# Performance work log

Measured on AMD Instinct MI355X. Metric: run time of the kernel, lower is better.

## Reference

```python
import jax, jax.numpy as jnp
import numpy as np

NUM_HEADS = 16
SRC_FACTS = 4


def setup_inputs() -> dict:
    key = jax.random.key(0)
    k1, k2, k3, k4, k5 = jax.random.split(key, 5)
    B, S, H, Dh = 16, 512, NUM_HEADS, 64  # B = batch(4) * src_facts(4)
    D = H * Dh  # d_model = 1024
    pre_q = jax.random.normal(k1, (B, S, H, Dh), dtype=jnp.float32)
    pre_v = jax.random.normal(k2, (B, S, H, Dh), dtype=jnp.float32)
    pre_k = jax.random.normal(k3, (B, S, H, Dh), dtype=jnp.float32)
    attn_mask = jax.random.randint(k4, (B, S, S), 0, 2).astype(jnp.int32)
    output_weights = jax.random.normal(k5, (D, D), dtype=jnp.float32) / np.float32(np.sqrt(D))
    return {
        "pre_q": pre_q,
        "pre_v": pre_v,
        "pre_k": pre_k,
        "attn_mask": attn_mask,
        "output_weights": output_weights,
        "out_seq_len": 512,
        "d_model": 1024,
    }


def reference(pre_q, pre_v, pre_k, attn_mask, output_weights, out_seq_len, d_model):
    B, Sq, H, Dh = pre_q.shape
    # Original: K.sqrt(cast(d_model) // num_heads) -> sqrt(head_dim)
    scale = jnp.sqrt(jnp.float32(float(d_model) // H))
    mask = attn_mask.astype(jnp.float32)[:, None]  # (B, 1, q, k) broadcast over heads
    # scores: (B, H, q, k)
    scores = jnp.einsum("bqhd,bkhd->bhqk", pre_q, pre_k) / scale
    # multiplicative pre-mask + additive -1e9 on masked slots
    scores = scores * mask + (1.0 - mask) * jnp.float32(-1e9)
    # softmax then multiplicative post-mask
    attn = jax.nn.softmax(scores, axis=-1) * mask
    heads = jnp.einsum("bhqk,bkhd->bqhd", attn, pre_v)  # (B, q, H, Dh)
    out = heads.reshape(B, Sq, H * Dh) @ output_weights  # (B, q, d_model)
    return out.reshape(-1, SRC_FACTS, out_seq_len, d_model)
```

## Files before the change

### kernel.cpp

```cpp
#include <hip/hip_runtime.h>
#include <hip/hip_bf16.h>


typedef __bf16 bf16;
typedef bf16 bf16x8 __attribute__((ext_vector_type(8)));
typedef bf16 bf16x4 __attribute__((ext_vector_type(4)));
typedef float floatx4 __attribute__((ext_vector_type(4)));
typedef float floatx16 __attribute__((ext_vector_type(16)));
typedef unsigned short ushort8 __attribute__((ext_vector_type(8)));
typedef unsigned long long u64;

#define MFMA32(A, B, C)    __builtin_amdgcn_mfma_f32_16x16x32_bf16((A), (B), (C), 0, 0, 0)
#define MFMA32x32(A, B, C) __builtin_amdgcn_mfma_f32_32x32x16_bf16((A), (B), (C), 0, 0, 0)

namespace {
constexpr int S    = 512;
constexpr int H    = 16;
constexpr int Dh   = 64;
constexpr int D    = 1024;
constexpr int LDT  = 72;
constexpr int LDTV = 136;
constexpr size_t QN = (size_t)16 * S * H * Dh;
constexpr size_t WN = (size_t)D * D;
}

__device__ __forceinline__ float fexp2(float x) {
#if defined(__HIP_DEVICE_COMPILE__) && __has_builtin(__builtin_amdgcn_exp2f)
    return __builtin_amdgcn_exp2f(x);
#else
    return exp2f(x);
#endif
}

__device__ __forceinline__ int sbfe1(unsigned bits, int bit) {
    return ((int)(bits << (31 - bit))) >> 31;
}

__device__ __forceinline__ void gload16(const bf16* g, bf16* ldsbase, int lane) {
#if __has_builtin(__builtin_amdgcn_global_load_lds)
    __builtin_amdgcn_global_load_lds(
        (__attribute__((address_space(1))) void*)(g),
        (__attribute__((address_space(3))) void*)(ldsbase), 16, 0, 0);
#else
    *(ushort8*)(ldsbase + lane * 8) = *(const ushort8*)g;
#endif
}

__global__ __launch_bounds__(256)
void prep_kernel(const float* __restrict__ Kf, const float* __restrict__ Vf,
                 const float* __restrict__ Wf, const int* __restrict__ Mg,
                 bf16* __restrict__ Kc, bf16* __restrict__ Vt,
                 bf16* __restrict__ Wt, u64* __restrict__ MB)
{
    __shared__ bf16 Ts[64 * LDT];
    const int blk = blockIdx.x, tid = threadIdx.x;

    if (blk < 1024) {
        const int c0 = blk * 1024 + tid;
        floatx4 f[4][2];
#pragma unroll
        for (int k = 0; k < 4; ++k) {
            const float* fs = Kf + (size_t)(c0 + k * 256) * 8;
            f[k][0] = *(const floatx4*)fs;
            f[k][1] = *(const floatx4*)(fs + 4);
        }
#pragma unroll
        for (int k = 0; k < 4; ++k) {
            bf16x8 v;
#pragma unroll
            for (int j = 0; j < 4; ++j) {
                v[j]     = (bf16)f[k][0][j];
                v[j + 4] = (bf16)f[k][1][j];
            }
            *(bf16x8*)(Kc + (size_t)(c0 + k * 256) * 8) = v;
        }
    } else if (blk < 3072) {
        const int bk2 = blk - 1024;
        const int bh  = bk2 >> 3, st = bk2 & 7;
        const int b   = bh >> 4, h = bh & 15;
        const int r   = tid >> 2, c = (tid & 3) * 16;
        const float* src = Vf + ((size_t)((b * S + st * 64 + r) * H + h)) * Dh + c;
        floatx4 f0 = *(const floatx4*)src;
        floatx4 f1 = *(const floatx4*)(src + 4);
        floatx4 f2 = *(const floatx4*)(src + 8);
        floatx4 f3 = *(const floatx4*)(src + 12);
#pragma unroll
        for (int i = 0; i < 4; ++i) {
            Ts[(c + i)      * LDT + (r ^ ((c + i)      & 48))] = (bf16)f0[i];
            Ts[(c + 4 + i)  * LDT + (r ^ ((c + 4 + i)  & 48))] = (bf16)f1[i];
            Ts[(c + 8 + i)  * LDT + (r ^ ((c + 8 + i)  & 48))] = (bf16)f2[i];
            Ts[(c + 12 + i) * LDT + (r ^ ((c + 12 + i) & 48))] = (bf16)f3[i];
        }
        __syncthreads();
        bf16* dst = Vt + ((size_t)bh * 64 + r) * S + st * 64 + c;
        const int rb = r * LDT + (c ^ (r & 48));
        *(ushort8*)dst       = *(const ushort8*)&Ts[rb];
        *(ushort8*)(dst + 8) = *(const ushort8*)&Ts[rb + 8];
    } else if (blk < 3328) {
        const int bk2 = blk - 3072;
        const int nb  = bk2 & 15, kb = bk2 >> 4;
        const int r   = tid >> 2, c = (tid & 3) * 16;
        const float* src = Wf + (size_t)(kb * 64 + r) * D + nb * 64 + c;
        floatx4 f0 = *(const floatx4*)src;
        floatx4 f1 = *(const floatx4*)(src + 4);
        floatx4 f2 = *(const floatx4*)(src + 8);
        floatx4 f3 = *(const floatx4*)(src + 12);
#pragma unroll
        for (int i = 0; i < 4; ++i) {
            Ts[(c + i)      * LDT + (r ^ ((c + i)      & 48))] = (bf16)f0[i];
            Ts[(c + 4 + i)  * LDT + (r ^ ((c + 4 + i)  & 48))] = (bf16)f1[i];
            Ts[(c + 8 + i)  * LDT + (r ^ ((c + 8 + i)  & 48))] = (bf16)f2[i];
            Ts[(c + 12 + i) * LDT + (r ^ ((c + 12 + i) & 48))] = (bf16)f3[i];
        }
        __syncthreads();
        bf16* dst = Wt + (size_t)(nb * 64 + r) * D + kb * 64 + c;
        const int rb = r * LDT + (c ^ (r & 48));
        *(ushort8*)dst       = *(const ushort8*)&Ts[rb];
        *(ushort8*)(dst + 8) = *(const ushort8*)&Ts[rb + 8];
    } else {
        const int bk2  = blk - 3328;
        const int lane = tid & 63;
        const int wv   = tid >> 6;
        const int u0   = bk2 * 16 + wv * 4;
        int mv[4][4];
#pragma unroll
        for (int u = 0; u < 4; ++u) {
            const int idx4 = u0 + u;
            const int row = idx4 >> 1, hf = idx4 & 1;
#pragma unroll
            for (int r = 0; r < 4; ++r)
                mv[u][r] = Mg[(size_t)row * 512 + hf * 256 + r * 64 + lane];
        }
#pragma unroll
        for (int u = 0; u < 4; ++u) {
            const int idx4 = u0 + u;
            const int row = idx4 >> 1, hf = idx4 & 1;
#pragma unroll
            for (int r = 0; r < 4; ++r) {
                u64 bm = __ballot(mv[u][r] != 0);
                if (lane == 0) MB[(size_t)row * 8 + hf * 4 + r] = bm;
            }
        }
    }
}

__global__ __launch_bounds__(256, 4)
void attn_kernel(const float* __restrict__ Qg, const bf16* __restrict__ Kc,
                 const bf16* __restrict__ Vtg, const u64* __restrict__ MB,
                 bf16* __restrict__ heads)
{
    __shared__ bf16 Ks[128 * LDT];
    __shared__ bf16 Vs[64 * LDTV];

    const int tid  = threadIdx.x;
    const int lane = tid & 63;
    const int wave = tid >> 6;
    const int l31  = lane & 31;
    const int half = lane >> 5;

    const int blk = blockIdx.x;
    const int h   = blk & 15;
    const int qt  = (blk >> 4) & 3;
    const int b   = blk >> 6;
    const int qw  = qt * 128 + wave * 32;

    constexpr float QSCL = 0.125f * 1.44269504088896340736f;
    bf16x8 aq[4];
    {
        const float* qb = Qg + ((size_t)((b * S + qw + l31) * H + h)) * Dh + half * 8;
#pragma unroll
        for (int ds = 0; ds < 4; ++ds) {
            floatx4 f0 = *(const floatx4*)(qb + ds * 16);
            floatx4 f1 = *(const floatx4*)(qb + ds * 16 + 4);
#pragma unroll
            for (int j = 0; j < 4; ++j) {
                aq[ds][j]     = (bf16)(f0[j] * QSCL);
                aq[ds][j + 4] = (bf16)(f1[j] * QSCL);
            }
        }
    }

    float rsum = 0.f;
    floatx16 O[2];
#pragma unroll
    for (int dt = 0; dt < 2; ++dt)
#pragma unroll
        for (int i = 0; i < 16; ++i) O[dt][i] = 0.f;

    const u64* mbrow = MB + ((size_t)b * S + qw + l31) * 8;
    const bf16* vplane = Vtg + (size_t)(b * 16 + h) * 64 * S;

    const int kr = tid >> 1, kc = (tid & 1) * 32;
    const int kp = (kr & ~12) | ((kr & 4) << 1) | ((kr & 8) >> 1);
    const int dr = tid >> 2, dc = (tid & 3) * 32;

    for (int it = 0; it < 4; ++it) {
        const int kb = it * 128;
        const bf16* ksrc = Kc + ((size_t)((b * S + kb + kp) * H + h)) * Dh + kc;
        const bf16* vsrc = vplane + (size_t)dr * S + kb + dc;
        ushort8 k0 = *(const ushort8*)ksrc;
        ushort8 k1 = *(const ushort8*)(ksrc + 8);
        ushort8 k2 = *(const ushort8*)(ksrc + 16);
        ushort8 k3 = *(const ushort8*)(ksrc + 24);
        ushort8 v0 = *(const ushort8*)vsrc;
        ushort8 v1 = *(const ushort8*)(vsrc + 8);
        ushort8 v2 = *(const ushort8*)(vsrc + 16);
        ushort8 v3 = *(const ushort8*)(vsrc + 24);
        u64 mA = mbrow[it * 2];
        u64 mC = mbrow[it * 2 + 1];

        __syncthreads();
        *(ushort8*)&Ks[kr * LDT + kc]       = k0;
        *(ushort8*)&Ks[kr * LDT + kc + 8]   = k1;
        *(ushort8*)&Ks[kr * LDT + kc + 16]  = k2;
        *(ushort8*)&Ks[kr * LDT + kc + 24]  = k3;
        *(ushort8*)&Vs[dr * LDTV + dc]      = v0;
        *(ushort8*)&Vs[dr * LDTV + dc + 8]  = v1;
        *(ushort8*)&Vs[dr * LDTV + dc + 16] = v2;
        *(ushort8*)&Vs[dr * LDTV + dc + 24] = v3;
        __syncthreads();

        bf16x8 pB[8];
#pragma unroll
        for (int t = 0; t < 4; ++t) {
            floatx16 acc;
#pragma unroll
            for (int i = 0; i < 16; ++i) acc[i] = 0.f;
#pragma unroll
            for (int ds = 0; ds < 4; ++ds) {
                bf16x8 ak = *(const bf16x8*)&Ks[(t * 32 + l31) * LDT + ds * 16 + half * 8];
                acc = MFMA32x32(ak, aq[ds], acc);
            }
            const u64 mw = (t < 2) ? mA : mC;
            const unsigned w = (unsigned)(mw >> ((t & 1) * 32 + half * 8));
#pragma unroll
            for (int r = 0; r < 16; ++r) {
                float e = fexp2(acc[r]);
                int sx = sbfe1(w, (r >> 3) * 16 + (r & 7));
                float p = __uint_as_float(__float_as_uint(e) & (unsigned)sx);
                rsum += p;
                pB[t * 2 + (r >> 3)][r & 7] = (bf16)p;
            }
        }

#pragma unroll
        for (int dt = 0; dt < 2; ++dt)
#pragma unroll
            for (int s_ = 0; s_ < 8; ++s_) {
                bf16x8 av = *(const bf16x8*)&Vs[(dt * 32 + l31) * LDTV + s_ * 16 + half * 8];
                O[dt] = MFMA32x32(av, pB[s_], O[dt]);
            }
    }

    rsum += __shfl_xor(rsum, 32, 64);
    const float inv = (rsum > 0.f) ? (1.f / rsum) : 0.f;

    bf16* hrow = heads + ((size_t)((b * S + qw + l31) * H + h)) * Dh;
#pragma unroll
    for (int dt = 0; dt < 2; ++dt) {
#pragma unroll
        for (int g = 0; g < 4; ++g) {
            bf16x4 h4;
#pragma unroll
            for (int j = 0; j < 4; ++j) h4[j] = (bf16)(O[dt][g * 4 + j] * inv);
            *(bf16x4*)&hrow[dt * 32 + g * 8 + half * 4] = h4;
        }
    }
}

__global__ __launch_bounds__(256)
void proj_kernel(const bf16* __restrict__ A, const bf16* __restrict__ Wt,
                 float* __restrict__ out)
{
    __shared__ bf16 As[128 * 32];
    __shared__ bf16 Ws[128 * 32];

    const int tid  = threadIdx.x;
    const int lane = tid & 63;
    const int wave = tid >> 6;
    const int l15  = lane & 15;
    const int quad = lane >> 4;

    const int nb = blockIdx.x & 7;
    const int mb = blockIdx.x >> 3;
    const int mbase = mb * 128, nbase = nb * 128;
    const int wm = (wave & 1) * 64, wn = (wave >> 1) * 64;

    const int ch0  = wave * 2;
    const int srow = lane >> 2;
    const int scol = (lane & 3) * 8;

    floatx4 O[4][4];
#pragma unroll
    for (int mt = 0; mt < 4; ++mt)
#pragma unroll
        for (int nt = 0; nt < 4; ++nt) O[mt][nt] = floatx4{0.f, 0.f, 0.f, 0.f};

    for (int kt = 0; kt < 32; ++kt) {
        const int kb = kt * 32;
        if (kt) __syncthreads();

        gload16(A  + (size_t)(mbase + ch0 * 16      + srow) * D + kb + scol, As + ch0 * 512,       lane);
        gload16(A  + (size_t)(mbase + (ch0 + 1) * 16 + srow) * D + kb + scol, As + (ch0 + 1) * 512, lane);
        gload16(Wt + (size_t)(nbase + ch0 * 16      + srow) * D + kb + scol, Ws + ch0 * 512,       lane);
        gload16(Wt + (size_t)(nbase + (ch0 + 1) * 16 + srow) * D + kb + scol, Ws + (ch0 + 1) * 512, lane);

        __syncthreads();

        bf16x8 fa[4];
#pragma unroll
        for (int mt = 0; mt < 4; ++mt)
            fa[mt] = *(const bf16x8*)&As[(wm + mt * 16 + l15) * 32 + quad * 8];
#pragma unroll
        for (int nt = 0; nt < 4; ++nt) {
            bf16x8 fb = *(const bf16x8*)&Ws[(wn + nt * 16 + l15) * 32 + quad * 8];
#pragma unroll
            for (int mt = 0; mt < 4; ++mt)
                O[mt][nt] = MFMA32(fa[mt], fb, O[mt][nt]);
        }
    }

#pragma unroll
    for (int mt = 0; mt < 4; ++mt) {
#pragma unroll
        for (int nt = 0; nt < 4; ++nt) {
#pragma unroll
            for (int reg = 0; reg < 4; ++reg) {
                const int m = mbase + wm + mt * 16 + quad * 4 + reg;
                const int n = nbase + wn + nt * 16 + l15;
                out[(size_t)m * D + n] = O[mt][nt][reg];
            }
        }
    }
}

extern "C" void kernel_launch(void* const* d_in, const int* in_sizes, int n_in,
                              void* d_out, int out_size, void* d_ws, size_t ws_size,
                              hipStream_t stream)
{
    const float* pre_q = (const float*)d_in[0];
    const float* pre_v = (const float*)d_in[1];
    const float* pre_k = (const float*)d_in[2];
    const int*   mask  = (const int*)d_in[3];
    const float* Wg    = (const float*)d_in[4];
    float* out = (float*)d_out;

    bf16* Kc    = (bf16*)d_ws;
    bf16* Vt    = Kc + QN;
    bf16* Wt    = Vt + QN;
    bf16* heads = Wt + WN;
    u64*  MB    = (u64*)(heads + QN);

    prep_kernel<<<4352, 256, 0, stream>>>(pre_k, pre_v, Wg, mask, Kc, Vt, Wt, MB);
    attn_kernel<<<1024, 256, 0, stream>>>(pre_q, Kc, Vt, MB, heads);
    proj_kernel<<<512, 256, 0, stream>>>(heads, Wt, out);
}
```

Baseline: 210.6 us.

## Restructure attention into single-wave blocks with 32-key tiles

Attention now launches one 64-thread wave per block over 4096 blocks instead of four waves per block sharing 128-key K/V tiles. Each iteration stages only a 32-key K tile and a 64x32 V tile in LDS and loops 16 times. The aim is smaller LDS per block, higher occupancy and cheaper single-wave barriers. In exchange, K/V tiles are no longer shared across four query waves, so global and L2 traffic for K/V rises roughly fourfold and there are more, smaller iterations.

After: 225.1 us. +6.8%, slower.

```diff
diff --git a/kernel.cpp b/kernel.cpp
--- a/kernel.cpp
+++ b/kernel.cpp
@@ -19,7 +19,7 @@
 constexpr int Dh   = 64;
 constexpr int D    = 1024;
 constexpr int LDT  = 72;
-constexpr int LDTV = 136;
+constexpr int LDTV = 40;
 constexpr size_t QN = (size_t)16 * S * H * Dh;
 constexpr size_t WN = (size_t)D * D;
 }
@@ -144,25 +144,23 @@
     }
 }
 
-__global__ __launch_bounds__(256, 4)
+__global__ __launch_bounds__(64, 4)
 void attn_kernel(const float* __restrict__ Qg, const bf16* __restrict__ Kc,
                  const bf16* __restrict__ Vtg, const u64* __restrict__ MB,
                  bf16* __restrict__ heads)
 {
-    __shared__ bf16 Ks[128 * LDT];
+    __shared__ bf16 Ks[32 * LDT];
     __shared__ bf16 Vs[64 * LDTV];
 
-    const int tid  = threadIdx.x;
-    const int lane = tid & 63;
-    const int wave = tid >> 6;
+    const int lane = threadIdx.x & 63;
     const int l31  = lane & 31;
     const int half = lane >> 5;
 
     const int blk = blockIdx.x;
     const int h   = blk & 15;
-    const int qt  = (blk >> 4) & 3;
-    const int b   = blk >> 6;
-    const int qw  = qt * 128 + wave * 32;
+    const int qt  = (blk >> 4) & 15;
+    const int b   = blk >> 8;
+    const int qw  = qt * 32;
 
     constexpr float QSCL = 0.125f * 1.44269504088896340736f;
     bf16x8 aq[4];
@@ -190,63 +188,57 @@
     const u64* mbrow = MB + ((size_t)b * S + qw + l31) * 8;
     const bf16* vplane = Vtg + (size_t)(b * 16 + h) * 64 * S;
 
-    const int kr = tid >> 1, kc = (tid & 1) * 32;
-    const int kp = (kr & ~12) | ((kr & 4) << 1) | ((kr & 8) >> 1);
-    const int dr = tid >> 2, dc = (tid & 3) * 32;
-
-    for (int it = 0; it < 4; ++it) {
-        const int kb = it * 128;
+    const int kr = lane >> 1, kc = (lane & 1) * 32;
+    const int kp = (kr & 0x13) | ((kr & 4) << 1) | ((kr & 8) >> 1);
+    const int vr = lane >> 2, vc = (lane & 3) * 8;
+
+    for (int it = 0; it < 16; ++it) {
+        const int kb = it * 32;
         const bf16* ksrc = Kc + ((size_t)((b * S + kb + kp) * H + h)) * Dh + kc;
-        const bf16* vsrc = vplane + (size_t)dr * S + kb + dc;
         ushort8 k0 = *(const ushort8*)ksrc;
         ushort8 k1 = *(const ushort8*)(ksrc + 8);
         ushort8 k2 = *(const ushort8*)(ksrc + 16);
         ushort8 k3 = *(const ushort8*)(ksrc + 24);
-        ushort8 v0 = *(const ushort8*)vsrc;
-        ushort8 v1 = *(const ushort8*)(vsrc + 8);
-        ushort8 v2 = *(const ushort8*)(vsrc + 16);
-        ushort8 v3 = *(const ushort8*)(vsrc + 24);
-        u64 mA = mbrow[it * 2];
-        u64 mC = mbrow[it * 2 + 1];
-
-        __syncthreads();
-        *(ushort8*)&Ks[kr * LDT + kc]       = k0;
-        *(ushort8*)&Ks[kr * LDT + kc + 8]   = k1;
-        *(ushort8*)&Ks[kr * LDT + kc + 16]  = k2;
-        *(ushort8*)&Ks[kr * LDT + kc + 24]  = k3;
-        *(ushort8*)&Vs[dr * LDTV + dc]      = v0;
-        *(ushort8*)&Vs[dr * LDTV + dc + 8]  = v1;
-        *(ushort8*)&Vs[dr * LDTV + dc + 16] = v2;
-        *(ushort8*)&Vs[dr * LDTV + dc + 24] = v3;
-        __syncthreads();
-
-        bf16x8 pB[8];
-#pragma unroll
-        for (int t = 0; t < 4; ++t) {
-            floatx16 acc;
-#pragma unroll
-            for (int i = 0; i < 16; ++i) acc[i] = 0.f;
-#pragma unroll
-            for (int ds = 0; ds < 4; ++ds) {
-                bf16x8 ak = *(const bf16x8*)&Ks[(t * 32 + l31) * LDT + ds * 16 + half * 8];
-                acc = MFMA32x32(ak, aq[ds], acc);
-            }
-            const u64 mw = (t < 2) ? mA : mC;
-            const unsigned w = (unsigned)(mw >> ((t & 1) * 32 + half * 8));
-#pragma unroll
-            for (int r = 0; r < 16; ++r) {
-                float e = fexp2(acc[r]);
-                int sx = sbfe1(w, (r >> 3) * 16 + (r & 7));
-                float p = __uint_as_float(__float_as_uint(e) & (unsigned)sx);
-                rsum += p;
-                pB[t * 2 + (r >> 3)][r & 7] = (bf16)p;
-            }
+        ushort8 v0 = *(const ushort8*)(vplane + (size_t)vr        * S + kb + vc);
+        ushort8 v1 = *(const ushort8*)(vplane + (size_t)(vr + 16) * S + kb + vc);
+        ushort8 v2 = *(const ushort8*)(vplane + (size_t)(vr + 32) * S + kb + vc);
+        ushort8 v3 = *(const ushort8*)(vplane + (size_t)(vr + 48) * S + kb + vc);
+        const u64 m64 = mbrow[it >> 1];
+
+        __syncthreads();
+        *(ushort8*)&Ks[kr * LDT + kc]        = k0;
+        *(ushort8*)&Ks[kr * LDT + kc + 8]    = k1;
+        *(ushort8*)&Ks[kr * LDT + kc + 16]   = k2;
+        *(ushort8*)&Ks[kr * LDT + kc + 24]   = k3;
+        *(ushort8*)&Vs[vr * LDTV + vc]        = v0;
+        *(ushort8*)&Vs[(vr + 16) * LDTV + vc] = v1;
+        *(ushort8*)&Vs[(vr + 32) * LDTV + vc] = v2;
+        *(ushort8*)&Vs[(vr + 48) * LDTV + vc] = v3;
+        __syncthreads();
+
+        floatx16 acc;
+#pragma unroll
+        for (int i = 0; i < 16; ++i) acc[i] = 0.f;
+#pragma unroll
+        for (int ds = 0; ds < 4; ++ds) {
+            bf16x8 ak = *(const bf16x8*)&Ks[l31 * LDT + ds * 16 + half * 8];
+            acc = MFMA32x32(ak, aq[ds], acc);
+        }
+        const unsigned w = (unsigned)(m64 >> ((it & 1) * 32 + half * 8));
+        bf16x8 pB[2];
+#pragma unroll
+        for (int r = 0; r < 16; ++r) {
+            float e = fexp2(acc[r]);
+            int sx = sbfe1(w, (r >> 3) * 16 + (r & 7));
+            float p = __uint_as_float(__float_as_uint(e) & (unsigned)sx);
+            rsum += p;
+            pB[r >> 3][r & 7] = (bf16)p;
         }
 
 #pragma unroll
         for (int dt = 0; dt < 2; ++dt)
 #pragma unroll
-            for (int s_ = 0; s_ < 8; ++s_) {
+            for (int s_ = 0; s_ < 2; ++s_) {
                 bf16x8 av = *(const bf16x8*)&Vs[(dt * 32 + l31) * LDTV + s_ * 16 + half * 8];
                 O[dt] = MFMA32x32(av, pB[s_], O[dt]);
             }
@@ -352,6 +344,6 @@
     u64*  MB    = (u64*)(heads + QN);
 
     prep_kernel<<<4352, 256, 0, stream>>>(pre_k, pre_v, Wg, mask, Kc, Vt, Wt, MB);
-    attn_kernel<<<1024, 256, 0, stream>>>(pre_q, Kc, Vt, MB, heads);
+    attn_kernel<<<4096, 64, 0, stream>>>(pre_q, Kc, Vt, MB, heads);
     proj_kernel<<<512, 256, 0, stream>>>(heads, Wt, out);
 }
```
